# Kernel optimization log

Hardware: AMD Instinct MI355X
Metric: run time of the kernel (lower is better)

Reference implementation:

```python
import jax, jax.numpy as jnp
import numpy as np

B, N, M = 4, 1024, 2048
D, H, HD, L, V = 768, 6, 128, 3, 4096
PEH = 64
FF = 4 * D
TEMP0 = 15.5


def _rms(x, w):
    return x * jax.lax.rsqrt(jnp.mean(x * x, axis=-1, keepdims=True) + 1e-8) * w


def _l2(x):
    n = jnp.sqrt(jnp.sum(x * x, axis=-1, keepdims=True))
    return x / jnp.maximum(n, 1e-12)


def setup_inputs():
    key = jax.random.key(0)
    it = iter(jax.random.split(key, 32))

    def rn(shape, s=0.02):
        return jax.random.normal(next(it), shape, jnp.float32) * s

    inp = {}
    inp['tokens'] = jax.random.randint(next(it), (B, N), 0, V)
    inp['acoustic'] = jax.random.normal(next(it), (B, M, D), jnp.float32)
    inp['embed'] = rn((V, D))
    inp['pe_freq'] = rn((PEH // 2,), 1.0)
    inp['pe_w'] = rn((PEH, D))
    inp['pe_b'] = jnp.zeros((D,), jnp.float32)
    inp['dpb_w0'] = rn((1, 64), 0.5)
    inp['dpb_b0'] = jnp.zeros((64,), jnp.float32)
    inp['dpb_w1'] = rn((64, 64), 0.1)
    inp['dpb_b1'] = jnp.zeros((64,), jnp.float32)
    inp['dpb_w2'] = rn((64, H), 0.1)
    inp['dpb_b2'] = jnp.zeros((H,), jnp.float32)
    inp['acoustic_norm_w'] = jnp.ones((D,), jnp.float32)
    inp['norm1'] = jnp.ones((L, D), jnp.float32)
    inp['norm2'] = jnp.ones((L, D), jnp.float32)
    inp['norm3'] = jnp.ones((L, D), jnp.float32)
    inp['sa_qkv'] = rn((L, D, 3 * H * HD))
    inp['sa_out'] = rn((L, H * HD, D))
    inp['temp'] = jnp.full((L,), TEMP0, jnp.float32)
    inp['ca_q'] = rn((L, D, H * HD))
    inp['ca_kv'] = rn((L, D, 2 * H * HD))
    inp['ca_out'] = rn((L, H * HD, D))
    inp['ff_w1'] = rn((L, D, FF))
    inp['ff_w2'] = rn((L, FF, D))
    inp['final_norm_w'] = jnp.ones((D,), jnp.float32)
    inp['out_w'] = rn((D, V))
    inp['out_b'] = jnp.zeros((V,), jnp.float32)
    return inp


def reference(tokens, acoustic, embed, pe_freq, pe_w, pe_b, dpb_w0, dpb_b0, dpb_w1, dpb_b1, dpb_w2, dpb_b2, acoustic_norm_w, norm1, norm2, norm3, sa_qkv, sa_out, temp, ca_q, ca_kv, ca_out, ff_w1, ff_w2, final_norm_w, out_w, out_b):
    x = embed[tokens]  # [B,N,D]
    # learnable fourier positional encoding (hidden_dim=64)
    p = jnp.arange(N, dtype=jnp.float32)[:, None]
    feat = jnp.concatenate([jnp.cos(p * pe_freq), jnp.sin(p * pe_freq)], axis=-1) / jnp.sqrt(jnp.float32(PEH))
    x = x + (feat @ pe_w + pe_b)

    # DynamicPositionBias: MLP over relative distance -> [H,N,N]
    dist = jnp.arange(-(N - 1), N, dtype=jnp.float32)[:, None]  # [2N-1,1]
    hmlp = jax.nn.silu(dist @ dpb_w0 + dpb_b0)
    hmlp = jax.nn.silu(hmlp @ dpb_w1 + dpb_b1)
    table = hmlp @ dpb_w2 + dpb_b2  # [2N-1, H]
    i = jnp.arange(N)
    rel = i[None, :] - i[:, None] + (N - 1)  # [N,N]
    pos_bias = jnp.transpose(table[rel], (2, 0, 1))  # [H,N,N]
    causal = i[None, :] > i[:, None]  # True where key index > query index
    neg = -jnp.finfo(jnp.float32).max

    xkv = _rms(acoustic, acoustic_norm_w)  # acoustic_norm applied once

    for l in range(L):
        # --- cosine-sim causal self-attention with temperature + pos bias ---
        hx = _rms(x, norm1[l])
        qkv = (hx @ sa_qkv[l]).reshape(B, N, H, HD, 3)  # 'b n (h d qkv)'
        q = jnp.transpose(qkv[..., 0], (0, 2, 1, 3))  # [B,H,N,HD]
        k = jnp.transpose(qkv[..., 1], (0, 2, 1, 3))
        v = jnp.transpose(qkv[..., 2], (0, 2, 1, 3))
        q, k = _l2(q), _l2(k)
        dots = jnp.einsum('bhid,bhjd->bhij', q, k) * temp[l] + pos_bias
        dots = jnp.where(causal, neg, dots)
        attn = jax.nn.softmax(dots, axis=-1)
        o = jnp.einsum('bhij,bhjd->bhid', attn, v)
        o = jnp.transpose(o, (0, 2, 1, 3)).reshape(B, N, H * HD)
        x = x + o @ sa_out[l]

        # --- cross attention to acoustic features (flash-attn math, scale 1/sqrt(d)) ---
        hx = _rms(x, norm2[l])
        q = (hx @ ca_q[l]).reshape(B, N, H, HD)
        kv = (xkv @ ca_kv[l]).reshape(B, M, H, HD, 2)  # 'b n (h d kv)'
        k, v = kv[..., 0], kv[..., 1]
        dots = jnp.einsum('bihd,bjhd->bhij', q, k) / jnp.sqrt(jnp.float32(HD))
        attn = jax.nn.softmax(dots, axis=-1)
        o = jnp.einsum('bhij,bjhd->bihd', attn, v).reshape(B, N, H * HD)
        x = x + o @ ca_out[l]

        # --- feed-forward: linear -> gelu -> linear ---
        hx = _rms(x, norm3[l])
        x = x + jax.nn.gelu(hx @ ff_w1[l], approximate=True) @ ff_w2[l]

    logits = _rms(x, final_norm_w) @ out_w + out_b  # [B,N,V]
    return logits
```

## Files before the change

kernel.cpp:

```cpp
#include <hip/hip_runtime.h>
#include <hip/hip_bf16.h>
#include <math.h>
#include <stddef.h>

#define Bc 4
#define Nc 1024
#define Mc 2048
#define Dc 768
#define Hc 6
#define HDc 128
#define Lc 3
#define Vc 4096
#define FFc 3072

typedef short bf16x8 __attribute__((ext_vector_type(8)));
typedef float f32x4 __attribute__((ext_vector_type(4)));
typedef ushort usx4 __attribute__((ext_vector_type(4)));

__device__ __forceinline__ float gelu_tanh(float x) {
    float x3 = x * x * x;
    return 0.5f * x * (1.0f + tanhf(0.7978845608028654f * (x + 0.044715f * x3)));
}
__device__ __forceinline__ float silu_f(float x) {
    return x / (1.0f + expf(-x));
}
__device__ __forceinline__ ushort f2bf(float x) {
    unsigned u = __float_as_uint(x);
    unsigned r = (u + 0x7fffu + ((u >> 16) & 1u)) >> 16;
    return (ushort)r;
}
__device__ __forceinline__ float bf2f(ushort u) {
    return __uint_as_float(((unsigned)u) << 16);
}
__device__ __forceinline__ void gl2lds16(const ushort* g, ushort* l) {
    __builtin_amdgcn_global_load_lds(
        (const __attribute__((address_space(1))) unsigned int*)(g),
        (__attribute__((address_space(3))) unsigned int*)(l),
        16, 0, 0);
}

__global__ __launch_bounds__(256) void pos_pe_kernel(
    const float* __restrict__ freq, const float* __restrict__ pe_w,
    const float* __restrict__ pe_b, float* __restrict__ pos)
{
    int n = blockIdx.x;
    __shared__ float feat[64];
    int tid = threadIdx.x;
    if (tid < 64) {
        float f;
        if (tid < 32) f = cosf((float)n * freq[tid]);
        else          f = sinf((float)n * freq[tid - 32]);
        feat[tid] = f * 0.125f;
    }
    __syncthreads();
    for (int d = tid; d < Dc; d += 256) {
        float s = pe_b[d];
#pragma unroll
        for (int h = 0; h < 64; ++h) s += feat[h] * pe_w[h * Dc + d];
        pos[(size_t)n * Dc + d] = s;
    }
}

__global__ __launch_bounds__(256) void embed_kernel(
    const int* __restrict__ tokens, const float* __restrict__ embed_w,
    const float* __restrict__ pos, float* __restrict__ x)
{
    size_t idx = (size_t)blockIdx.x * 256 + threadIdx.x;
    if (idx >= (size_t)Bc * Nc * Dc) return;
    int d  = (int)(idx % Dc);
    size_t bn = idx / Dc;
    int n  = (int)(bn % Nc);
    int tok = tokens[bn];
    x[idx] = embed_w[(size_t)tok * Dc + d] + pos[(size_t)n * Dc + d];
}

__global__ __launch_bounds__(64) void dpb_kernel(
    const float* __restrict__ w0, const float* __restrict__ b0,
    const float* __restrict__ w1, const float* __restrict__ b1,
    const float* __restrict__ w2, const float* __restrict__ b2,
    float* __restrict__ table)
{
    int r = blockIdx.x;
    int j = threadIdx.x;
    float dist = (float)r - (float)(Nc - 1);
    __shared__ float s0[64], s1[64];
    s0[j] = silu_f(dist * w0[j] + b0[j]);
    __syncthreads();
    float a = b1[j];
#pragma unroll 8
    for (int k = 0; k < 64; ++k) a += s0[k] * w1[k * 64 + j];
    s1[j] = silu_f(a);
    __syncthreads();
    if (j < Hc) {
        float t = b2[j];
#pragma unroll 8
        for (int k = 0; k < 64; ++k) t += s1[k] * w2[k * Hc + j];
        table[(size_t)r * Hc + j] = t;
    }
}

__global__ __launch_bounds__(256) void rms_kernel(
    const float* __restrict__ in, const float* __restrict__ w,
    ushort* __restrict__ out)
{
    size_t row = blockIdx.x;
    const float* rp = in + row * Dc;
    ushort* op = out + row * Dc;
    int tid = threadIdx.x;
    float4 v = make_float4(0.f, 0.f, 0.f, 0.f);
    float s = 0.f;
    int d4 = tid << 2;
    if (tid < 192) {
        v = *(const float4*)&rp[d4];
        s = v.x * v.x + v.y * v.y + v.z * v.z + v.w * v.w;
    }
    __shared__ float red[256];
    red[tid] = s;
    __syncthreads();
    for (int o = 128; o > 0; o >>= 1) {
        if (tid < o) red[tid] += red[tid + o];
        __syncthreads();
    }
    float rs = rsqrtf(red[0] * (1.0f / Dc) + 1e-8f);
    if (tid < 192) {
        float4 wv = *(const float4*)&w[d4];
        usx4 pk;
        pk.x = f2bf(v.x * rs * wv.x); pk.y = f2bf(v.y * rs * wv.y);
        pk.z = f2bf(v.z * rs * wv.z); pk.w = f2bf(v.w * rs * wv.w);
        *(usx4*)&op[d4] = pk;
    }
}

__global__ __launch_bounds__(256) void rms_reduce_kernel(
    float* __restrict__ x, const float* __restrict__ P, int nsplit, size_t MN,
    const float* __restrict__ w, ushort* __restrict__ out)
{
    size_t row = blockIdx.x;
    float* xp = x + row * Dc;
    ushort* op = out + row * Dc;
    int tid = threadIdx.x;
    int d4 = tid << 2;
    float4 v = make_float4(0.f, 0.f, 0.f, 0.f);
    float s = 0.f;
    if (tid < 192) {
        v = *(const float4*)&xp[d4];
        for (int z = 0; z < nsplit; ++z) {
            float4 p = *(const float4*)&P[(size_t)z * MN + row * Dc + d4];
            v.x += p.x; v.y += p.y; v.z += p.z; v.w += p.w;
        }
        *(float4*)&xp[d4] = v;
        s = v.x * v.x + v.y * v.y + v.z * v.z + v.w * v.w;
    }
    __shared__ float red[256];
    red[tid] = s;
    __syncthreads();
    for (int o = 128; o > 0; o >>= 1) {
        if (tid < o) red[tid] += red[tid + o];
        __syncthreads();
    }
    float rs = rsqrtf(red[0] * (1.0f / Dc) + 1e-8f);
    if (tid < 192) {
        float4 wv = *(const float4*)&w[d4];
        usx4 pk;
        pk.x = f2bf(v.x * rs * wv.x); pk.y = f2bf(v.y * rs * wv.y);
        pk.z = f2bf(v.z * rs * wv.z); pk.w = f2bf(v.w * rs * wv.w);
        *(usx4*)&op[d4] = pk;
    }
}

__global__ __launch_bounds__(256) void wt_kernel(
    const float* __restrict__ in, ushort* __restrict__ out, int K_, int N_)
{
    int n0 = blockIdx.x << 6, k0 = blockIdx.y << 6;
    __shared__ ushort t[64][65];
    int tid = threadIdx.x;
    int r = tid >> 4, c4 = (tid & 15) << 2;
    for (int rr = r; rr < 64; rr += 16) {
        float4 v = *(const float4*)&in[(size_t)(k0 + rr) * N_ + n0 + c4];
        t[rr][c4]     = f2bf(v.x);
        t[rr][c4 + 1] = f2bf(v.y);
        t[rr][c4 + 2] = f2bf(v.z);
        t[rr][c4 + 3] = f2bf(v.w);
    }
    __syncthreads();
    int nr = tid >> 2, cw = (tid & 3) << 4;
    ushort tmp[16];
#pragma unroll
    for (int j = 0; j < 16; ++j) tmp[j] = t[cw + j][nr];
#pragma unroll
    for (int s = 0; s < 2; ++s)
        *(bf16x8*)&out[(size_t)(n0 + nr) * K_ + k0 + cw + (s << 3)] =
            *(const bf16x8*)&tmp[s << 3];
}

__global__ __launch_bounds__(256) void gemm_bf16_kernel(
    const ushort* __restrict__ A, const ushort* __restrict__ Bt,
    const float* __restrict__ bias, const float* __restrict__ res,
    float* __restrict__ Cf, ushort* __restrict__ Cb,
    int M_, int N_, int K_, int act, int ksplit)
{
    __shared__ __align__(16) ushort sraw[2 * 2 * 8 * 512];
    ushort* As = sraw;
    ushort* Bs = sraw + 2 * 8 * 512;
    int m0 = blockIdx.y << 7, n0 = blockIdx.x << 7;
    int tid = threadIdx.x;
    int wave = tid >> 6, lane = tid & 63;
    int li = lane & 15, lq = lane >> 4;
    int wm = (wave >> 1) << 6, wn = (wave & 1) << 6;

    int kchunk = K_ / ksplit;
    int kbeg = blockIdx.z * kchunk;
    int niter = kchunk >> 5;

    f32x4 acc[4][4];
#pragma unroll
    for (int i = 0; i < 4; ++i)
#pragma unroll
        for (int j = 0; j < 4; ++j) {
            acc[i][j][0] = 0.f; acc[i][j][1] = 0.f;
            acc[i][j][2] = 0.f; acc[i][j][3] = 0.f;
        }

    auto stage = [&](int buf, int k0) {
#pragma unroll
        for (int i = 0; i < 2; ++i) {
            int fb = (wave << 1) + i;
            const ushort* ga = A  + (size_t)(m0 + (fb << 4) + li) * K_ + k0 + (lq << 3);
            const ushort* gb = Bt + (size_t)(n0 + (fb << 4) + li) * K_ + k0 + (lq << 3);
            gl2lds16(ga, &As[(buf << 12) + (fb << 9)]);
            gl2lds16(gb, &Bs[(buf << 12) + (fb << 9)]);
        }
    };

    stage(0, kbeg);
    __syncthreads();

    for (int it = 0; it < niter; ++it) {
        int cur = it & 1;
        if (it + 1 < niter) stage(cur ^ 1, kbeg + ((it + 1) << 5));
        bf16x8 af[4], bfr[4];
#pragma unroll
        for (int t = 0; t < 4; ++t) {
            af[t]  = *(const bf16x8*)&As[(cur << 12) + (((wm >> 4) + t) << 9) + (lane << 3)];
            bfr[t] = *(const bf16x8*)&Bs[(cur << 12) + (((wn >> 4) + t) << 9) + (lane << 3)];
        }
#pragma unroll
        for (int mt = 0; mt < 4; ++mt)
#pragma unroll
            for (int nt = 0; nt < 4; ++nt)
                acc[mt][nt] = __builtin_amdgcn_mfma_f32_16x16x32_bf16(
                    af[mt], bfr[nt], acc[mt][nt], 0, 0, 0);
        __syncthreads();
    }

    float* lt = (float*)sraw;
    float* dstF = Cf;
    if (ksplit > 1) dstF = Cf + (size_t)blockIdx.z * M_ * N_;

#pragma unroll
    for (int half = 0; half < 2; ++half) {
        __syncthreads();
        if ((wm >> 6) == half) {
#pragma unroll
            for (int mt = 0; mt < 4; ++mt) {
#pragma unroll
                for (int r = 0; r < 4; ++r) {
                    int lrow = (mt << 4) + (lq << 2) + r;
                    int grow = m0 + (half << 6) + lrow;
#pragma unroll
                    for (int nt = 0; nt < 4; ++nt) {
                        int col = wn + (nt << 4) + li;
                        float v = acc[mt][nt][r];
                        if (ksplit == 1) {
                            int gcol = n0 + col;
                            if (bias) v += bias[gcol];
                            if (act == 1) v = gelu_tanh(v);
                            if (res) v += res[(size_t)grow * N_ + gcol];
                        }
                        lt[(lrow << 7) + col] = v;
                    }
                }
            }
        }
        __syncthreads();
        if (Cb) {
            int lrow = tid >> 4;
            int c8 = (tid & 15) << 3;
#pragma unroll
            for (int p = 0; p < 4; ++p) {
                int row = (p << 4) + lrow;
                f32x4 a = *(const f32x4*)&lt[(row << 7) + c8];
                f32x4 b = *(const f32x4*)&lt[(row << 7) + c8 + 4];
                union { bf16x8 v; ushort u[8]; } pk;
#pragma unroll
                for (int j = 0; j < 4; ++j) {
                    pk.u[j] = f2bf(a[j]);
                    pk.u[4 + j] = f2bf(b[j]);
                }
                int grow = m0 + (half << 6) + row;
                *(bf16x8*)&Cb[(size_t)grow * N_ + n0 + c8] = pk.v;
            }
        } else {
            int lrow = tid >> 5;
            int c4 = (tid & 31) << 2;
#pragma unroll
            for (int p = 0; p < 8; ++p) {
                int row = (p << 3) + lrow;
                f32x4 a = *(const f32x4*)&lt[(row << 7) + c4];
                int grow = m0 + (half << 6) + row;
                *(f32x4*)&dstF[(size_t)grow * N_ + n0 + c4] = a;
            }
        }
    }
}

__global__ __launch_bounds__(128) void unpack_sa_kernel(
    const ushort* __restrict__ qkv, ushort* __restrict__ qo,
    ushort* __restrict__ ko, ushort* __restrict__ vo)
{
    int bid = blockIdx.x;
    int h = bid % Hc;
    int bn = bid / Hc;
    int b = bn / Nc, n = bn % Nc;
    int d = threadIdx.x;
    size_t base = (size_t)bn * (3 * Hc * HDc) + (size_t)(h * HDc + d) * 3;
    float q = bf2f(qkv[base]), k = bf2f(qkv[base + 1]);
    ushort v = qkv[base + 2];
    __shared__ float rq[128], rk[128];
    rq[d] = q * q; rk[d] = k * k;
    __syncthreads();
    for (int o = 64; o > 0; o >>= 1) {
        if (d < o) { rq[d] += rq[d + o]; rk[d] += rk[d + o]; }
        __syncthreads();
    }
    float qn = fmaxf(sqrtf(rq[0]), 1e-12f);
    float kn = fmaxf(sqrtf(rk[0]), 1e-12f);
    size_t oidx = (((size_t)(b * Hc + h) * Nc) + n) * HDc + d;
    qo[oidx] = f2bf(q / qn);
    ko[oidx] = f2bf(k / kn);
    vo[oidx] = v;
}

__global__ __launch_bounds__(256) void unpack_caq_red_kernel(
    const float* __restrict__ P, ushort* __restrict__ qo)
{
    size_t idx = (size_t)blockIdx.x * 256 + threadIdx.x;
    if (idx >= (size_t)Bc * Hc * Nc * HDc) return;
    int d = (int)(idx & (HDc - 1));
    size_t t = idx >> 7;
    int n = (int)(t % Nc); t /= Nc;
    int h = (int)(t % Hc); int b = (int)(t / Hc);
    const size_t MNq = (size_t)Bc * Nc * (Hc * HDc);
    size_t src = ((size_t)(b * Nc + n)) * (Hc * HDc) + h * HDc + d;
    qo[idx] = f2bf(P[src] + P[MNq + src]);
}

__global__ __launch_bounds__(256) void unpack_cakv_kernel(
    const ushort* __restrict__ in, ushort* __restrict__ ko, ushort* __restrict__ vo)
{
    size_t idx = (size_t)blockIdx.x * 256 + threadIdx.x;
    if (idx >= (size_t)Bc * Hc * Mc * HDc) return;
    int d = (int)(idx & (HDc - 1));
    size_t t = idx >> 7;
    int m = (int)(t % Mc); t /= Mc;
    int h = (int)(t % Hc); int b = (int)(t / Hc);
    size_t src = ((size_t)(b * Mc + m)) * (2 * Hc * HDc) + (size_t)(h * HDc + d) * 2;
    ko[idx] = in[src];
    vo[idx] = in[src + 1];
}

__global__ __launch_bounds__(256) void transpose_kernel(
    const ushort* __restrict__ in, ushort* __restrict__ out, int R)
{
    int bh = blockIdx.z;
    int r0 = blockIdx.x << 6, d0 = blockIdx.y << 6;
    const ushort* ip = in + (size_t)bh * R * HDc;
    ushort* op = out + (size_t)bh * HDc * R;
    __shared__ ushort tile[64][66];
    int t = threadIdx.x;
    int lr = t >> 5, lc = (t & 31) << 1;
    for (int rr = lr; rr < 64; rr += 8) {
        ushort2 v = *(const ushort2*)&ip[(size_t)(r0 + rr) * HDc + d0 + lc];
        tile[rr][lc] = v.x; tile[rr][lc + 1] = v.y;
    }
    __syncthreads();
    for (int dd = lr; dd < 64; dd += 8) {
        ushort2 v;
        v.x = tile[lc][dd]; v.y = tile[lc + 1][dd];
        *(ushort2*)&op[(size_t)(d0 + dd) * R + r0 + lc] = v;
    }
}

__global__ __launch_bounds__(256) void attn_mfma_kernel(
    const ushort* __restrict__ Qg, const ushort* __restrict__ Kg,
    const ushort* __restrict__ VTg, ushort* __restrict__ O,
    int NQ, int NK, float scale_const, const float* __restrict__ scale_ptr,
    const float* __restrict__ bias_table, int causal)
{
    int qtiles = NQ >> 6;
    int qt = blockIdx.x % qtiles;
    int bh = blockIdx.x / qtiles;
    int h = bh % Hc, b = bh / Hc;
    int q0 = qt << 6;

    const ushort* Qb = Qg + (size_t)bh * NQ * HDc;
    const ushort* Kb = Kg + (size_t)bh * NK * HDc;
    const ushort* Vb = VTg + (size_t)bh * HDc * NK;

    float scale = scale_const * (scale_ptr ? scale_ptr[0] : 1.0f);

    __shared__ __align__(16) ushort Ks[2][16 * 512];
    __shared__ __align__(16) ushort Vs[2][16 * 512];
    __shared__ __align__(16) ushort Ps[4][16][72];
    __shared__ float bias_s[2][128];

    int tid = threadIdx.x;
    int wave = tid >> 6, lane = tid & 63;
    int li = lane & 15, lq = lane >> 4;
    int qrel = (wave << 4) + li;

    bf16x8 qfrag[4];
    {
        const ushort* qrow = Qb + (size_t)(q0 + qrel) * HDc + (lq << 3);
#pragma unroll
        for (int kt = 0; kt < 4; ++kt)
            qfrag[kt] = *(const bf16x8*)&qrow[kt << 5];
    }

    f32x4 oacc[8];
#pragma unroll
    for (int i = 0; i < 8; ++i) { oacc[i][0] = 0.f; oacc[i][1] = 0.f; oacc[i][2] = 0.f; oacc[i][3] = 0.f; }
    float m_run = -INFINITY, l_run = 0.f;

    auto stage_kv = [&](int buf, int jt) {
        int j0 = jt << 6;
#pragma unroll
        for (int i = 0; i < 4; ++i) {
            int f = (wave << 2) + i;
            int mt = f >> 2, kt = f & 3;
            const ushort* gk = Kb + (size_t)(j0 + (mt << 4) + li) * HDc + (kt << 5) + (lq << 3);
            gl2lds16(gk, &Ks[buf][f << 9]);
            int dt = f >> 1, s = f & 1;
            const ushort* gv = Vb + (size_t)((dt << 4) + li) * NK + j0 + (s << 5) + (lq << 3);
            gl2lds16(gv, &Vs[buf][f << 9]);
        }
        if (bias_table && tid < 127)
            bias_s[buf][tid] = bias_table[(size_t)(j0 - q0 - 63 + Nc - 1 + tid) * Hc + h];
    };

    int jt_end = causal ? (q0 >> 6) + 1 : (NK >> 6);

    stage_kv(0, 0);
    __syncthreads();

    for (int jt = 0; jt < jt_end; ++jt) {
        int cur = jt & 1;
        if (jt + 1 < jt_end) stage_kv(cur ^ 1, jt + 1);
        int j0 = jt << 6;

        f32x4 sacc[4];
#pragma unroll
        for (int mt = 0; mt < 4; ++mt) {
            f32x4 s; s[0] = 0.f; s[1] = 0.f; s[2] = 0.f; s[3] = 0.f;
#pragma unroll
            for (int kt = 0; kt < 4; ++kt) {
                bf16x8 kf = *(const bf16x8*)&Ks[cur][(((mt << 2) + kt) << 9) + (lane << 3)];
                s = __builtin_amdgcn_mfma_f32_16x16x32_bf16(kf, qfrag[kt], s, 0, 0, 0);
            }
            sacc[mt] = s;
        }

        float sv[4][4];
        float mtile = -INFINITY;
#pragma unroll
        for (int mt = 0; mt < 4; ++mt)
#pragma unroll
            for (int r = 0; r < 4; ++r) {
                int jrel = (mt << 4) + (lq << 2) + r;
                float sx = sacc[mt][r] * scale;
                if (bias_table) sx += bias_s[cur][jrel - qrel + 63];
                if (causal && (j0 + jrel) > (q0 + qrel)) sx = -INFINITY;
                sv[mt][r] = sx;
                mtile = fmaxf(mtile, sx);
            }
        mtile = fmaxf(mtile, __shfl_xor(mtile, 16));
        mtile = fmaxf(mtile, __shfl_xor(mtile, 32));
        float m_new = fmaxf(m_run, mtile);
        float alpha = __expf(m_run - m_new);
        m_run = m_new;
        float ps = 0.f;
#pragma unroll
        for (int mt = 0; mt < 4; ++mt)
#pragma unroll
            for (int r = 0; r < 4; ++r) {
                float p = __expf(sv[mt][r] - m_new);
                sv[mt][r] = p;
                ps += p;
            }
        ps += __shfl_xor(ps, 16);
        ps += __shfl_xor(ps, 32);
        l_run = l_run * alpha + ps;

#pragma unroll
        for (int mt = 0; mt < 4; ++mt) {
            usx4 pk;
            pk.x = f2bf(sv[mt][0]); pk.y = f2bf(sv[mt][1]);
            pk.z = f2bf(sv[mt][2]); pk.w = f2bf(sv[mt][3]);
            *(usx4*)&Ps[wave][li][(mt << 4) + (lq << 2)] = pk;
        }

        float ar[4];
#pragma unroll
        for (int r = 0; r < 4; ++r) ar[r] = __shfl(alpha, (lq << 2) + r);
#pragma unroll
        for (int dt = 0; dt < 8; ++dt)
#pragma unroll
            for (int r = 0; r < 4; ++r) oacc[dt][r] *= ar[r];

        bf16x8 pf0 = *(const bf16x8*)&Ps[wave][li][(lq << 3)];
        bf16x8 pf1 = *(const bf16x8*)&Ps[wave][li][32 + (lq << 3)];
#pragma unroll
        for (int dt = 0; dt < 8; ++dt) {
            bf16x8 v0 = *(const bf16x8*)&Vs[cur][(((dt << 1) + 0) << 9) + (lane << 3)];
            bf16x8 v1 = *(const bf16x8*)&Vs[cur][(((dt << 1) + 1) << 9) + (lane << 3)];
            oacc[dt] = __builtin_amdgcn_mfma_f32_16x16x32_bf16(pf0, v0, oacc[dt], 0, 0, 0);
            oacc[dt] = __builtin_amdgcn_mfma_f32_16x16x32_bf16(pf1, v1, oacc[dt], 0, 0, 0);
        }
        __syncthreads();
    }

#pragma unroll
    for (int r = 0; r < 4; ++r) {
        float linv = 1.0f / __shfl(l_run, (lq << 2) + r);
        int gq = q0 + (wave << 4) + (lq << 2) + r;
        ushort* op = O + ((size_t)(b * NQ + gq)) * (Hc * HDc) + h * HDc;
#pragma unroll
        for (int dt = 0; dt < 8; ++dt)
            op[(dt << 4) + li] = f2bf(oacc[dt][r] * linv);
    }
}

static inline void launch_gemm(const ushort* A, const ushort* Bt, const float* bias,
                               const float* res, float* Cf, ushort* Cb,
                               int M_, int N_, int K_, int act, int ksplit,
                               hipStream_t s)
{
    dim3 g(N_ / 128, M_ / 128, ksplit);
    hipLaunchKernelGGL(gemm_bf16_kernel, g, dim3(256), 0, s,
                       A, Bt, bias, res, Cf, Cb, M_, N_, K_, act, ksplit);
}

extern "C" void kernel_launch(void* const* d_in, const int* in_sizes, int n_in,
                              void* d_out, int out_size, void* d_ws, size_t ws_size,
                              hipStream_t stream)
{
    const int*   tokens   = (const int*)  d_in[0];
    const float* acoustic = (const float*)d_in[1];
    const float* embed_w  = (const float*)d_in[2];
    const float* pe_freq  = (const float*)d_in[3];
    const float* pe_w     = (const float*)d_in[4];
    const float* pe_b     = (const float*)d_in[5];
    const float* dpb_w0   = (const float*)d_in[6];
    const float* dpb_b0   = (const float*)d_in[7];
    const float* dpb_w1   = (const float*)d_in[8];
    const float* dpb_b1   = (const float*)d_in[9];
    const float* dpb_w2   = (const float*)d_in[10];
    const float* dpb_b2   = (const float*)d_in[11];
    const float* ac_nw    = (const float*)d_in[12];
    const float* norm1    = (const float*)d_in[13];
    const float* norm2    = (const float*)d_in[14];
    const float* norm3    = (const float*)d_in[15];
    const float* sa_qkv   = (const float*)d_in[16];
    const float* sa_out_w = (const float*)d_in[17];
    const float* temp     = (const float*)d_in[18];
    const float* ca_q_w   = (const float*)d_in[19];
    const float* ca_kv_w  = (const float*)d_in[20];
    const float* ca_out_w = (const float*)d_in[21];
    const float* ff_w1    = (const float*)d_in[22];
    const float* ff_w2    = (const float*)d_in[23];
    const float* fin_nw   = (const float*)d_in[24];
    const float* out_w    = (const float*)d_in[25];
    const float* out_b    = (const float*)d_in[26];
    float* out = (float*)d_out;

    const size_t SZ_X   = (size_t)Bc * Nc * Dc;
    const size_t SZ_POS = (size_t)Nc * Dc;
    const size_t SZ_TAB = 16384;
    const size_t SZ_XKV = (size_t)Bc * Mc * Dc;
    const size_t SZ_BIG = (size_t)Bc * Nc * FFc;
    const size_t SZ_QH  = (size_t)Bc * Hc * Nc * HDc;
    const size_t SZ_KH  = (size_t)Bc * Hc * Mc * HDc;

    float* ws = (float*)d_ws;
    float* x     = ws;
    float* pos   = x + SZ_X;
    float* table = pos + SZ_POS;
    ushort* hx    = (ushort*)(table + SZ_TAB);
    ushort* xkvb  = hx + SZ_X;
    ushort* attnO = xkvb + SZ_XKV;
    ushort* bigBb = attnO + SZ_X;
    ushort* qb    = bigBb + SZ_BIG;
    ushort* kb    = qb + SZ_QH;
    ushort* vb    = kb + SZ_KH;
    ushort* vTb   = vb + SZ_KH;
    ushort* wT    = vTb + SZ_KH;

    const size_t W_QKV = (size_t)Dc * 3 * Hc * HDc;
    const size_t W_O   = (size_t)Hc * HDc * Dc;
    const size_t W_CKV = (size_t)Dc * 2 * Hc * HDc;
    const size_t W_F   = (size_t)Dc * FFc;
    const size_t W_LAYER = W_QKV + 3 * W_O + W_CKV + 2 * W_F;
    ushort* outWT = wT + 3 * W_LAYER;

    float* Pq = (float*)qb;
    float* Pk = (float*)kb;
    const size_t MN = (size_t)Bc * Nc * Dc;

    const float CA_SCALE = 0.08838834764831843f;

    for (int l = 0; l < Lc; ++l) {
        ushort* wl = wT + (size_t)l * W_LAYER;
        ushort* qkvT = wl;
        ushort* soT  = qkvT + W_QKV;
        ushort* cqT  = soT + W_O;
        ushort* ckvT = cqT + W_O;
        ushort* coT  = ckvT + W_CKV;
        ushort* f1T  = coT + W_O;
        ushort* f2T  = f1T + W_F;
        hipLaunchKernelGGL(wt_kernel, dim3(3 * Hc * HDc / 64, Dc / 64), dim3(256), 0, stream,
                           sa_qkv + (size_t)l * W_QKV, qkvT, Dc, 3 * Hc * HDc);
        hipLaunchKernelGGL(wt_kernel, dim3(Dc / 64, Hc * HDc / 64), dim3(256), 0, stream,
                           sa_out_w + (size_t)l * W_O, soT, Hc * HDc, Dc);
        hipLaunchKernelGGL(wt_kernel, dim3(Hc * HDc / 64, Dc / 64), dim3(256), 0, stream,
                           ca_q_w + (size_t)l * W_O, cqT, Dc, Hc * HDc);
        hipLaunchKernelGGL(wt_kernel, dim3(2 * Hc * HDc / 64, Dc / 64), dim3(256), 0, stream,
                           ca_kv_w + (size_t)l * W_CKV, ckvT, Dc, 2 * Hc * HDc);
        hipLaunchKernelGGL(wt_kernel, dim3(Dc / 64, Hc * HDc / 64), dim3(256), 0, stream,
                           ca_out_w + (size_t)l * W_O, coT, Hc * HDc, Dc);
        hipLaunchKernelGGL(wt_kernel, dim3(FFc / 64, Dc / 64), dim3(256), 0, stream,
                           ff_w1 + (size_t)l * W_F, f1T, Dc, FFc);
        hipLaunchKernelGGL(wt_kernel, dim3(Dc / 64, FFc / 64), dim3(256), 0, stream,
                           ff_w2 + (size_t)l * W_F, f2T, FFc, Dc);
    }
    hipLaunchKernelGGL(wt_kernel, dim3(Vc / 64, Dc / 64), dim3(256), 0, stream,
                       out_w, outWT, Dc, Vc);

    hipLaunchKernelGGL(pos_pe_kernel, dim3(Nc), dim3(256), 0, stream,
                       pe_freq, pe_w, pe_b, pos);
    hipLaunchKernelGGL(embed_kernel, dim3((unsigned)((SZ_X + 255) / 256)), dim3(256), 0, stream,
                       tokens, embed_w, pos, x);
    hipLaunchKernelGGL(dpb_kernel, dim3(2 * Nc - 1), dim3(64), 0, stream,
                       dpb_w0, dpb_b0, dpb_w1, dpb_b1, dpb_w2, dpb_b2, table);
    hipLaunchKernelGGL(rms_kernel, dim3(Bc * Mc), dim3(256), 0, stream,
                       acoustic, ac_nw, xkvb);

    for (int l = 0; l < Lc; ++l) {
        const float* n1 = norm1 + (size_t)l * Dc;
        const float* n2 = norm2 + (size_t)l * Dc;
        const float* n3 = norm3 + (size_t)l * Dc;
        ushort* wl = wT + (size_t)l * W_LAYER;
        ushort* qkvT = wl;
        ushort* soT  = qkvT + W_QKV;
        ushort* cqT  = soT + W_O;
        ushort* ckvT = cqT + W_O;
        ushort* coT  = ckvT + W_CKV;
        ushort* f1T  = coT + W_O;
        ushort* f2T  = f1T + W_F;

        if (l == 0)
            hipLaunchKernelGGL(rms_kernel, dim3(Bc * Nc), dim3(256), 0, stream, x, n1, hx);
        else
            hipLaunchKernelGGL(rms_reduce_kernel, dim3(Bc * Nc), dim3(256), 0, stream,
                               x, Pq, 3, MN, n1, hx);
        launch_gemm(hx, qkvT, nullptr, nullptr, nullptr, bigBb,
                    Bc * Nc, 3 * Hc * HDc, Dc, 0, 1, stream);
        hipLaunchKernelGGL(unpack_sa_kernel, dim3(Bc * Nc * Hc), dim3(128), 0, stream,
                           bigBb, qb, kb, vb);
        hipLaunchKernelGGL(transpose_kernel, dim3(Nc / 64, 2, Bc * Hc), dim3(256), 0, stream,
                           vb, vTb, Nc);
        hipLaunchKernelGGL(attn_mfma_kernel, dim3(Bc * Hc * (Nc / 64)), dim3(256), 0, stream,
                           qb, kb, vTb, attnO, Nc, Nc, 1.0f, temp + l, table, 1);
        launch_gemm(attnO, soT, nullptr, nullptr, Pq, nullptr,
                    Bc * Nc, Dc, Hc * HDc, 0, 3, stream);
        hipLaunchKernelGGL(rms_reduce_kernel, dim3(Bc * Nc), dim3(256), 0, stream,
                           x, Pq, 3, MN, n2, hx);

        launch_gemm(hx, cqT, nullptr, nullptr, Pk, nullptr,
                    Bc * Nc, Hc * HDc, Dc, 0, 2, stream);
        hipLaunchKernelGGL(unpack_caq_red_kernel, dim3((unsigned)((SZ_QH + 255) / 256)),
                           dim3(256), 0, stream, Pk, qb);
        launch_gemm(xkvb, ckvT, nullptr, nullptr, nullptr, bigBb,
                    Bc * Mc, 2 * Hc * HDc, Dc, 0, 1, stream);
        hipLaunchKernelGGL(unpack_cakv_kernel, dim3((unsigned)((SZ_KH + 255) / 256)), dim3(256),
                           0, stream, bigBb, kb, vb);
        hipLaunchKernelGGL(transpose_kernel, dim3(Mc / 64, 2, Bc * Hc), dim3(256), 0, stream,
                           vb, vTb, Mc);
        hipLaunchKernelGGL(attn_mfma_kernel, dim3(Bc * Hc * (Nc / 64)), dim3(256), 0, stream,
                           qb, kb, vTb, attnO, Nc, Mc, CA_SCALE, nullptr, nullptr, 0);
        launch_gemm(attnO, coT, nullptr, nullptr, Pq, nullptr,
                    Bc * Nc, Dc, Hc * HDc, 0, 3, stream);
        hipLaunchKernelGGL(rms_reduce_kernel, dim3(Bc * Nc), dim3(256), 0, stream,
                           x, Pq, 3, MN, n3, hx);

        launch_gemm(hx, f1T, nullptr, nullptr, nullptr, bigBb,
                    Bc * Nc, FFc, Dc, 1, 1, stream);
        launch_gemm(bigBb, f2T, nullptr, nullptr, Pq, nullptr,
                    Bc * Nc, Dc, FFc, 0, 3, stream);
    }

    hipLaunchKernelGGL(rms_reduce_kernel, dim3(Bc * Nc), dim3(256), 0, stream,
                       x, Pq, 3, MN, fin_nw, hx);
    launch_gemm(hx, outWT, out_b, nullptr, out, nullptr,
                Bc * Nc, Vc, Dc, 0, 1, stream);
}
```

Before: 1.914 ms.

## Use 8-wave GEMM blocks and XCD-aware block swizzle for GEMM and attention

The GEMM kernel now runs with 512 threads (8 waves) per 128x128 tile. Each wave computes a 64x32 sub-tile with half the accumulators and issues a single global-to-LDS load per operand per stage. Both the GEMM and attention kernels remap block IDs so that consecutive tiles land on the same XCD, which is meant to improve L2 locality across the MI355X's chiplets. The aim is more latency hiding per CU and better cache reuse. The cost is more LDS fragment reads per MFMA, since each wave now does a 4x2 rather than 4x4 MFMA grid per A/B fragment load.

```diff
diff --git a/kernel.cpp b/kernel.cpp
--- a/kernel.cpp
+++ b/kernel.cpp
@@ -37,6 +37,11 @@
         (const __attribute__((address_space(1))) unsigned int*)(g),
         (__attribute__((address_space(3))) unsigned int*)(l),
         16, 0, 0);
+}
+__device__ __forceinline__ int xcd_swz(int bid, int nwg) {
+    int q = nwg >> 3, r = nwg & 7;
+    int xcd = bid & 7, i = bid >> 3;
+    return (xcd < r ? xcd * (q + 1) : r * (q + 1) + (xcd - r) * q) + i;
 }
 
 __global__ __launch_bounds__(256) void pos_pe_kernel(
@@ -193,7 +198,7 @@
             *(const bf16x8*)&tmp[s << 3];
 }
 
-__global__ __launch_bounds__(256) void gemm_bf16_kernel(
+__global__ __launch_bounds__(512) void gemm_bf16_kernel(
     const ushort* __restrict__ A, const ushort* __restrict__ Bt,
     const float* __restrict__ bias, const float* __restrict__ res,
     float* __restrict__ Cf, ushort* __restrict__ Cb,
@@ -202,34 +207,36 @@
     __shared__ __align__(16) ushort sraw[2 * 2 * 8 * 512];
     ushort* As = sraw;
     ushort* Bs = sraw + 2 * 8 * 512;
-    int m0 = blockIdx.y << 7, n0 = blockIdx.x << 7;
+
+    int nwg = gridDim.x * gridDim.y;
+    int swz = xcd_swz(blockIdx.y * gridDim.x + blockIdx.x, nwg);
+    int n0 = (swz % gridDim.x) << 7;
+    int m0 = (swz / gridDim.x) << 7;
+
     int tid = threadIdx.x;
     int wave = tid >> 6, lane = tid & 63;
     int li = lane & 15, lq = lane >> 4;
-    int wm = (wave >> 1) << 6, wn = (wave & 1) << 6;
+    int wm = (wave >> 2) << 6;
+    int wn = (wave & 3) << 5;
 
     int kchunk = K_ / ksplit;
     int kbeg = blockIdx.z * kchunk;
     int niter = kchunk >> 5;
 
-    f32x4 acc[4][4];
+    f32x4 acc[4][2];
 #pragma unroll
     for (int i = 0; i < 4; ++i)
 #pragma unroll
-        for (int j = 0; j < 4; ++j) {
+        for (int j = 0; j < 2; ++j) {
             acc[i][j][0] = 0.f; acc[i][j][1] = 0.f;
             acc[i][j][2] = 0.f; acc[i][j][3] = 0.f;
         }
 
     auto stage = [&](int buf, int k0) {
-#pragma unroll
-        for (int i = 0; i < 2; ++i) {
-            int fb = (wave << 1) + i;
-            const ushort* ga = A  + (size_t)(m0 + (fb << 4) + li) * K_ + k0 + (lq << 3);
-            const ushort* gb = Bt + (size_t)(n0 + (fb << 4) + li) * K_ + k0 + (lq << 3);
-            gl2lds16(ga, &As[(buf << 12) + (fb << 9)]);
-            gl2lds16(gb, &Bs[(buf << 12) + (fb << 9)]);
-        }
+        const ushort* ga = A  + (size_t)(m0 + (wave << 4) + li) * K_ + k0 + (lq << 3);
+        const ushort* gb = Bt + (size_t)(n0 + (wave << 4) + li) * K_ + k0 + (lq << 3);
+        gl2lds16(ga, &As[(buf << 12) + (wave << 9)]);
+        gl2lds16(gb, &Bs[(buf << 12) + (wave << 9)]);
     };
 
     stage(0, kbeg);
@@ -238,16 +245,17 @@
     for (int it = 0; it < niter; ++it) {
         int cur = it & 1;
         if (it + 1 < niter) stage(cur ^ 1, kbeg + ((it + 1) << 5));
-        bf16x8 af[4], bfr[4];
-#pragma unroll
-        for (int t = 0; t < 4; ++t) {
+        bf16x8 af[4], bfr[2];
+#pragma unroll
+        for (int t = 0; t < 4; ++t)
             af[t]  = *(const bf16x8*)&As[(cur << 12) + (((wm >> 4) + t) << 9) + (lane << 3)];
+#pragma unroll
+        for (int t = 0; t < 2; ++t)
             bfr[t] = *(const bf16x8*)&Bs[(cur << 12) + (((wn >> 4) + t) << 9) + (lane << 3)];
-        }
 #pragma unroll
         for (int mt = 0; mt < 4; ++mt)
 #pragma unroll
-            for (int nt = 0; nt < 4; ++nt)
+            for (int nt = 0; nt < 2; ++nt)
                 acc[mt][nt] = __builtin_amdgcn_mfma_f32_16x16x32_bf16(
                     af[mt], bfr[nt], acc[mt][nt], 0, 0, 0);
         __syncthreads();
@@ -268,7 +276,7 @@
                     int lrow = (mt << 4) + (lq << 2) + r;
                     int grow = m0 + (half << 6) + lrow;
 #pragma unroll
-                    for (int nt = 0; nt < 4; ++nt) {
+                    for (int nt = 0; nt < 2; ++nt) {
                         int col = wn + (nt << 4) + li;
                         float v = acc[mt][nt][r];
                         if (ksplit == 1) {
@@ -287,8 +295,8 @@
             int lrow = tid >> 4;
             int c8 = (tid & 15) << 3;
 #pragma unroll
-            for (int p = 0; p < 4; ++p) {
-                int row = (p << 4) + lrow;
+            for (int p = 0; p < 2; ++p) {
+                int row = (p << 5) + lrow;
                 f32x4 a = *(const f32x4*)&lt[(row << 7) + c8];
                 f32x4 b = *(const f32x4*)&lt[(row << 7) + c8 + 4];
                 union { bf16x8 v; ushort u[8]; } pk;
@@ -304,8 +312,8 @@
             int lrow = tid >> 5;
             int c4 = (tid & 31) << 2;
 #pragma unroll
-            for (int p = 0; p < 8; ++p) {
-                int row = (p << 3) + lrow;
+            for (int p = 0; p < 4; ++p) {
+                int row = (p << 4) + lrow;
                 f32x4 a = *(const f32x4*)&lt[(row << 7) + c4];
                 int grow = m0 + (half << 6) + row;
                 *(f32x4*)&dstF[(size_t)grow * N_ + n0 + c4] = a;
@@ -398,8 +406,9 @@
     const float* __restrict__ bias_table, int causal)
 {
     int qtiles = NQ >> 6;
-    int qt = blockIdx.x % qtiles;
-    int bh = blockIdx.x / qtiles;
+    int bid = xcd_swz(blockIdx.x, gridDim.x);
+    int qt = bid % qtiles;
+    int bh = bid / qtiles;
     int h = bh % Hc, b = bh / Hc;
     int q0 = qt << 6;
 
@@ -546,7 +555,7 @@
                                hipStream_t s)
 {
     dim3 g(N_ / 128, M_ / 128, ksplit);
-    hipLaunchKernelGGL(gemm_bf16_kernel, g, dim3(256), 0, s,
+    hipLaunchKernelGGL(gemm_bf16_kernel, g, dim3(512), 0, s,
                        A, Bt, bias, res, Cf, Cb, M_, N_, K_, act, ksplit);
 }
 
```

Measured after the change: 1.822 ms. -4.8%, faster.
